# Kernel optimization log

Hardware: AMD Instinct MI355X
Metric: run time of the kernel (lower is better)

The kernel has to match this reference:

```python
import jax, jax.numpy as jnp
import numpy as np

SIGMA = 1e-4            # df_cone_height
PENALIZE_OUTSIDE = True
POINT2PLANE = False
EPS = 1e-12


def _tri_frame(tris):
    """tris: [..., 3, 3] -> centroid c [...,3], unit normal n [...,3], circum-radius r [...]."""
    v0, v1, v2 = tris[..., 0, :], tris[..., 1, :], tris[..., 2, :]
    c = (v0 + v1 + v2) / 3.0
    n = jnp.cross(v1 - v0, v2 - v0)
    n = n / jnp.maximum(jnp.linalg.norm(n, axis=-1, keepdims=True), EPS)
    r = jnp.sqrt(jnp.maximum(jnp.maximum(jnp.sum((v0 - c) ** 2, -1),
                                         jnp.sum((v1 - c) ** 2, -1)),
                             jnp.sum((v2 - c) ** 2, -1)))
    return c, n, r


def _cone_psi(points, c, n, r):
    """Conic distance-field value of each point w.r.t. a triangle cone.
    points: [..., 3, 3] (3 vertices), c/n: [..., 3], r: [...]. Returns [..., 3].
    Cone: axis = triangle normal through centroid, base radius r, height SIGMA.
    """
    u = points - c[..., None, :]                       # [..., 3v, 3]
    h = jnp.einsum('...vk,...k->...v', u, n)           # signed height along normal
    rho = jnp.linalg.norm(u - h[..., None] * n[..., None, :], axis=-1)  # radial dist
    radial = jnp.maximum(1.0 - rho / jnp.maximum(r[..., None], EPS), 0.0)
    if PENALIZE_OUTSIDE:
        axial = jnp.maximum(SIGMA - h, 0.0)            # also penalize thin band above surface
    else:
        axial = jnp.maximum(-h, 0.0)                   # only true penetration (below surface)
    return radial * axial


def setup_inputs() -> dict:
    key = jax.random.key(0)
    B, V, F, C = 8, 10475, 20908, 262144
    k1, k2, k3, k4 = jax.random.split(key, 4)
    vertices = jax.random.normal(k1, (B, V, 3), dtype=jnp.float32)
    faces = jax.random.randint(k2, (F, 3), 0, V)
    idxs = jax.random.randint(k3, (B, C, 2), 0, F)
    invalid = jax.random.uniform(k4, (B, C)) < 0.2     # padded (-1) collision slots
    collision_idxs = jnp.where(invalid[..., None], -1, idxs)
    return {"vertices": vertices, "faces": faces, "collision_idxs": collision_idxs}


def reference(vertices, faces, collision_idxs):
    # triangles: [B, F, 3, 3]
    triangles = jnp.take(vertices, faces, axis=1)
    recv_idx = collision_idxs[..., 0]                  # [B, C]
    intr_idx = collision_idxs[..., 1]
    valid = (recv_idx >= 0) & (intr_idx >= 0)
    # irregular gather of colliding triangle pairs: [B, C, 3, 3]
    recv = jnp.take_along_axis(triangles, jnp.clip(recv_idx, 0)[..., None, None], axis=1)
    intr = jnp.take_along_axis(triangles, jnp.clip(intr_idx, 0)[..., None, None], axis=1)
    rc, rn, rr = _tri_frame(recv)
    ic, inn, ir = _tri_frame(intr)
    psi_i = _cone_psi(intr, rc, rn, rr)                # intruder verts in receiver cone [B,C,3]
    psi_r = _cone_psi(recv, ic, inn, ir)               # receiver verts in intruder cone
    # penetration vector per vertex = -psi * n (unit normal) -> squared norm = psi^2
    per_pair = jnp.sum(psi_i ** 2 + psi_r ** 2, axis=-1)  # [B, C]
    loss = jnp.sum(jnp.where(valid, per_pair, 0.0), axis=1)  # [B]
    # original returns 0.0 when no collision index is >= 0
    return jnp.where(jnp.any(valid), loss, jnp.zeros_like(loss))
```

## Files before the change

### kernel.cpp

```cpp
#include <hip/hip_runtime.h>
#include <hip/hip_fp16.h>

#define SIGMA_C 1e-4f
#define EPS_C   1e-12f
#define BLOCK   256
#define GPT     4

struct V3 { float x, y, z; };

__device__ __forceinline__ V3 v3sub(V3 a, V3 b) { return {a.x - b.x, a.y - b.y, a.z - b.z}; }
__device__ __forceinline__ float v3dot(V3 a, V3 b) { return a.x * b.x + a.y * b.y + a.z * b.z; }
__device__ __forceinline__ V3 v3cross(V3 a, V3 b) {
    return {a.y * b.z - a.z * b.y,
            a.z * b.x - a.x * b.z,
            a.x * b.y - a.y * b.x};
}
__device__ __forceinline__ int imax0(int x) { return x > 0 ? x : 0; }

__device__ __forceinline__ void tri_frame(const V3 v[3], V3& c, V3& n, float& r) {
    const float third = 1.0f / 3.0f;
    c.x = (v[0].x + v[1].x + v[2].x) * third;
    c.y = (v[0].y + v[1].y + v[2].y) * third;
    c.z = (v[0].z + v[1].z + v[2].z) * third;
    V3 e1 = v3sub(v[1], v[0]);
    V3 e2 = v3sub(v[2], v[0]);
    n = v3cross(e1, e2);
    float nn = sqrtf(v3dot(n, n));
    float inv = 1.0f / fmaxf(nn, EPS_C);
    n.x *= inv; n.y *= inv; n.z *= inv;
    V3 d0 = v3sub(v[0], c), d1 = v3sub(v[1], c), d2 = v3sub(v[2], c);
    float m = fmaxf(fmaxf(v3dot(d0, d0), v3dot(d1, d1)), v3dot(d2, d2));
    r = sqrtf(m);
}

__device__ __forceinline__ float cone_psi2(const V3 p[3], V3 c, V3 n, float r) {
    float inv_r = 1.0f / fmaxf(r, EPS_C);
    float s = 0.0f;
#pragma unroll
    for (int i = 0; i < 3; ++i) {
        V3 u = v3sub(p[i], c);
        float h = v3dot(u, n);
        V3 w = {u.x - h * n.x, u.y - h * n.y, u.z - h * n.z};
        float rho = sqrtf(v3dot(w, w));
        float radial = fmaxf(1.0f - rho * inv_r, 0.0f);
        float axial = fmaxf(SIGMA_C - h, 0.0f);
        float psi = radial * axial;
        s += psi * psi;
    }
    return s;
}

union RecU { float4 f[2]; __half h[16]; };

__global__ void precompute_tri_h(const float* __restrict__ verts,
                                 const int*   __restrict__ faces,
                                 float4* __restrict__ table,
                                 float* __restrict__ out,
                                 int V, int F, int B) {
    if (blockIdx.x == 0 && threadIdx.x < (unsigned)B)
        out[threadIdx.x] = 0.0f;

    const int b = blockIdx.x % B;
    const int chunk = blockIdx.x / B;
    const int f = chunk * blockDim.x + threadIdx.x;
    if (f >= F) return;

    const float* vb = verts + (size_t)b * (size_t)V * 3u;
    int i0 = faces[3 * f + 0];
    int i1 = faces[3 * f + 1];
    int i2 = faces[3 * f + 2];
    V3 v[3];
    v[0] = {vb[3 * i0 + 0], vb[3 * i0 + 1], vb[3 * i0 + 2]};
    v[1] = {vb[3 * i1 + 0], vb[3 * i1 + 1], vb[3 * i1 + 2]};
    v[2] = {vb[3 * i2 + 0], vb[3 * i2 + 1], vb[3 * i2 + 2]};
    V3 c, n; float r;
    tri_frame(v, c, n, r);

    RecU u;
    u.h[0]  = __float2half(v[0].x); u.h[1]  = __float2half(v[0].y); u.h[2]  = __float2half(v[0].z);
    u.h[3]  = __float2half(v[1].x); u.h[4]  = __float2half(v[1].y); u.h[5]  = __float2half(v[1].z);
    u.h[6]  = __float2half(v[2].x); u.h[7]  = __float2half(v[2].y); u.h[8]  = __float2half(v[2].z);
    u.h[9]  = __float2half(c.x);    u.h[10] = __float2half(c.y);    u.h[11] = __float2half(c.z);
    u.h[12] = __float2half(n.x);    u.h[13] = __float2half(n.y);    u.h[14] = __float2half(n.z);
    u.h[15] = __float2half(r);

    float4* rec = table + ((size_t)b * F + f) * 2;
    rec[0] = u.f[0];
    rec[1] = u.f[1];
}

__device__ __forceinline__ void unpack_rec_h(float4 a, float4 b,
                                             V3 p[3], V3& c, V3& n, float& r) {
    RecU u; u.f[0] = a; u.f[1] = b;
    p[0] = {__half2float(u.h[0]),  __half2float(u.h[1]),  __half2float(u.h[2])};
    p[1] = {__half2float(u.h[3]),  __half2float(u.h[4]),  __half2float(u.h[5])};
    p[2] = {__half2float(u.h[6]),  __half2float(u.h[7]),  __half2float(u.h[8])};
    c = {__half2float(u.h[9]),  __half2float(u.h[10]), __half2float(u.h[11])};
    n = {__half2float(u.h[12]), __half2float(u.h[13]), __half2float(u.h[14])};
    r = __half2float(u.h[15]);
}

__device__ __forceinline__ void gather_group(const float4* __restrict__ tb, int4 q,
                                             float4 G[8], float w[2]) {
    w[0] = ((q.x | q.y) >= 0) ? 1.0f : 0.0f;
    w[1] = ((q.z | q.w) >= 0) ? 1.0f : 0.0f;
    const float4* R0 = tb + (size_t)imax0(q.x) * 2;
    const float4* I0 = tb + (size_t)imax0(q.y) * 2;
    const float4* R1 = tb + (size_t)imax0(q.z) * 2;
    const float4* I1 = tb + (size_t)imax0(q.w) * 2;
    G[0] = R0[0]; G[1] = R0[1];
    G[2] = I0[0]; G[3] = I0[1];
    G[4] = R1[0]; G[5] = R1[1];
    G[6] = I1[0]; G[7] = I1[1];
}

__device__ __forceinline__ float compute_pair(const float4 G0, const float4 G1,
                                              const float4 G2, const float4 G3, float w) {
    V3 rp[3], rc, rn; float rr;
    unpack_rec_h(G0, G1, rp, rc, rn, rr);
    V3 ip[3], ic, inn; float ir;
    unpack_rec_h(G2, G3, ip, ic, inn, ir);
    return w * (cone_psi2(ip, rc, rn, rr) + cone_psi2(rp, ic, inn, ir));
}

__device__ __forceinline__ float compute_group(const float4 G[8], const float w[2]) {
    return compute_pair(G[0], G[1], G[2], G[3], w[0]) +
           compute_pair(G[4], G[5], G[6], G[7], w[1]);
}

__global__ void __launch_bounds__(BLOCK)
pair_kernel_h(const float4* __restrict__ table,
              const int4*  __restrict__ coll4,
              float* __restrict__ out,
              int F, int C4, int B) {
    const int b = blockIdx.x % B;
    const int chunk = blockIdx.x / B;
    const int4* cb = coll4 + (size_t)b * C4;
    const float4* tb = table + (size_t)b * ((size_t)F * 2);

    const int base = chunk * (BLOCK * GPT) + threadIdx.x;

    float acc = 0.0f;
    float4 GA[8], GB[8];
    float wA[2], wB[2];
    int4 q_even, q_odd;

    {
        int g0 = base;
        int g1 = base + BLOCK;
        q_even = (g0 < C4) ? cb[g0] : make_int4(-1, -1, -1, -1);
        q_odd  = (GPT > 1 && g1 < C4) ? cb[g1] : make_int4(-1, -1, -1, -1);
        gather_group(tb, q_even, GA, wA);
    }

#pragma unroll
    for (int i = 0; i < GPT; ++i) {
        if ((i & 1) == 0) {
            if (i + 2 < GPT) {
                int g = base + (i + 2) * BLOCK;
                q_even = (g < C4) ? cb[g] : make_int4(-1, -1, -1, -1);
            }
            if (i + 1 < GPT)
                gather_group(tb, q_odd, GB, wB);
            acc += compute_group(GA, wA);
        } else {
            if (i + 2 < GPT) {
                int g = base + (i + 2) * BLOCK;
                q_odd = (g < C4) ? cb[g] : make_int4(-1, -1, -1, -1);
            }
            if (i + 1 < GPT)
                gather_group(tb, q_even, GA, wA);
            acc += compute_group(GB, wB);
        }
    }

#pragma unroll
    for (int off = 32; off > 0; off >>= 1)
        acc += __shfl_down(acc, off, 64);

    __shared__ float red[16];
    int lane = threadIdx.x & 63;
    int wid  = threadIdx.x >> 6;
    if (lane == 0) red[wid] = acc;
    __syncthreads();
    if (threadIdx.x == 0) {
        float s = 0.0f;
        int nw = blockDim.x >> 6;
        for (int i = 0; i < nw; ++i) s += red[i];
        atomicAdd(&out[b], s);
    }
}

__global__ void interp_zero(float* out, int n) {
    int i = blockIdx.x * blockDim.x + threadIdx.x;
    if (i < n) out[i] = 0.0f;
}

__global__ void pair_kernel_gather(const float* __restrict__ verts,
                                   const int*   __restrict__ faces,
                                   const int2*  __restrict__ coll,
                                   float* __restrict__ out,
                                   int V, int C) {
    const int b = blockIdx.y;
    const float* vb = verts + (size_t)b * (size_t)V * 3u;
    const int2* cb = coll + (size_t)b * (size_t)C;

    float acc = 0.0f;
    const int stride = gridDim.x * blockDim.x;
    for (int c = blockIdx.x * blockDim.x + threadIdx.x; c < C; c += stride) {
        int2 idx = cb[c];
        if ((idx.x | idx.y) >= 0) {
            const int* fr = faces + 3 * idx.x;
            const int* fi = faces + 3 * idx.y;
            V3 tr[3], ti[3];
#pragma unroll
            for (int j = 0; j < 3; ++j) {
                int vr = fr[j];
                tr[j] = {vb[3 * vr + 0], vb[3 * vr + 1], vb[3 * vr + 2]};
                int vi = fi[j];
                ti[j] = {vb[3 * vi + 0], vb[3 * vi + 1], vb[3 * vi + 2]};
            }
            V3 rc, rn; float rr;
            tri_frame(tr, rc, rn, rr);
            V3 ic, in_; float ir;
            tri_frame(ti, ic, in_, ir);
            acc += cone_psi2(ti, rc, rn, rr);
            acc += cone_psi2(tr, ic, in_, ir);
        }
    }

#pragma unroll
    for (int off = 32; off > 0; off >>= 1)
        acc += __shfl_down(acc, off, 64);

    __shared__ float red[16];
    int lane = threadIdx.x & 63;
    int wid  = threadIdx.x >> 6;
    if (lane == 0) red[wid] = acc;
    __syncthreads();
    if (threadIdx.x == 0) {
        float s = 0.0f;
        int nw = blockDim.x >> 6;
        for (int i = 0; i < nw; ++i) s += red[i];
        atomicAdd(&out[b], s);
    }
}

extern "C" void kernel_launch(void* const* d_in, const int* in_sizes, int n_in,
                              void* d_out, int out_size, void* d_ws, size_t ws_size,
                              hipStream_t stream) {
    const float* verts = (const float*)d_in[0];
    const int*   faces = (const int*)d_in[1];
    float* out = (float*)d_out;

    const int B = out_size;
    const int V = in_sizes[0] / (3 * B);
    const int F = in_sizes[1] / 3;
    const int C = in_sizes[2] / (2 * B);

    const size_t table_bytes = (size_t)B * (size_t)F * 32u;

    if (ws_size >= table_bytes && (C % 2) == 0) {
        float4* table = (float4*)d_ws;
        const int4* coll4 = (const int4*)d_in[2];
        const int C4 = C / 2;

        const int pchunks = (F + 255) / 256;
        precompute_tri_h<<<dim3(pchunks * B), dim3(256), 0, stream>>>(
            verts, faces, table, out, V, F, B);

        const int per_block = BLOCK * GPT;
        const int chunks = (C4 + per_block - 1) / per_block;
        pair_kernel_h<<<dim3(chunks * B), dim3(BLOCK), 0, stream>>>(
            table, coll4, out, F, C4, B);
    } else {
        const int2* coll = (const int2*)d_in[2];
        interp_zero<<<1, 64, 0, stream>>>(out, B);
        pair_kernel_gather<<<dim3(256, B), dim3(256), 0, stream>>>(
            verts, faces, coll, out, V, C);
    }
}
```

Measured before the change: 32.16 us.

## Stage triangle-record gathers into LDS with async global_load_lds double-buffering

Adds a new pair kernel where each wave issues direct global-to-LDS loads (global_load_lds) for the receiver and intruder triangle records of the next tile. It overlaps them with compute on the current tile, using manual vmcnt waits and a double buffer. The goal is to hide gather latency without holding many float4 registers, which should raise occupancy. The precompute kernel now handles two faces per thread. The new path runs only when C divides evenly by the per-block pair count, and it relies on hand-written waitcnt ordering being correct.

```diff
diff --git a/kernel.cpp b/kernel.cpp
--- a/kernel.cpp
+++ b/kernel.cpp
@@ -3,8 +3,8 @@
 
 #define SIGMA_C 1e-4f
 #define EPS_C   1e-12f
-#define BLOCK   256
-#define GPT     4
+#define WPB     4
+#define TILE_T  8
 
 struct V3 { float x, y, z; };
 
@@ -52,43 +52,6 @@
 
 union RecU { float4 f[2]; __half h[16]; };
 
-__global__ void precompute_tri_h(const float* __restrict__ verts,
-                                 const int*   __restrict__ faces,
-                                 float4* __restrict__ table,
-                                 float* __restrict__ out,
-                                 int V, int F, int B) {
-    if (blockIdx.x == 0 && threadIdx.x < (unsigned)B)
-        out[threadIdx.x] = 0.0f;
-
-    const int b = blockIdx.x % B;
-    const int chunk = blockIdx.x / B;
-    const int f = chunk * blockDim.x + threadIdx.x;
-    if (f >= F) return;
-
-    const float* vb = verts + (size_t)b * (size_t)V * 3u;
-    int i0 = faces[3 * f + 0];
-    int i1 = faces[3 * f + 1];
-    int i2 = faces[3 * f + 2];
-    V3 v[3];
-    v[0] = {vb[3 * i0 + 0], vb[3 * i0 + 1], vb[3 * i0 + 2]};
-    v[1] = {vb[3 * i1 + 0], vb[3 * i1 + 1], vb[3 * i1 + 2]};
-    v[2] = {vb[3 * i2 + 0], vb[3 * i2 + 1], vb[3 * i2 + 2]};
-    V3 c, n; float r;
-    tri_frame(v, c, n, r);
-
-    RecU u;
-    u.h[0]  = __float2half(v[0].x); u.h[1]  = __float2half(v[0].y); u.h[2]  = __float2half(v[0].z);
-    u.h[3]  = __float2half(v[1].x); u.h[4]  = __float2half(v[1].y); u.h[5]  = __float2half(v[1].z);
-    u.h[6]  = __float2half(v[2].x); u.h[7]  = __float2half(v[2].y); u.h[8]  = __float2half(v[2].z);
-    u.h[9]  = __float2half(c.x);    u.h[10] = __float2half(c.y);    u.h[11] = __float2half(c.z);
-    u.h[12] = __float2half(n.x);    u.h[13] = __float2half(n.y);    u.h[14] = __float2half(n.z);
-    u.h[15] = __float2half(r);
-
-    float4* rec = table + ((size_t)b * F + f) * 2;
-    rec[0] = u.f[0];
-    rec[1] = u.f[1];
-}
-
 __device__ __forceinline__ void unpack_rec_h(float4 a, float4 b,
                                              V3 p[3], V3& c, V3& n, float& r) {
     RecU u; u.f[0] = a; u.f[1] = b;
@@ -100,6 +63,145 @@
     r = __half2float(u.h[15]);
 }
 
+__device__ __forceinline__ float compute_pair(const float4 G0, const float4 G1,
+                                              const float4 G2, const float4 G3, float w) {
+    V3 rp[3], rc, rn; float rr;
+    unpack_rec_h(G0, G1, rp, rc, rn, rr);
+    V3 ip[3], ic, inn; float ir;
+    unpack_rec_h(G2, G3, ip, ic, inn, ir);
+    return w * (cone_psi2(ip, rc, rn, rr) + cone_psi2(rp, ic, inn, ir));
+}
+
+__device__ __forceinline__ void gload_lds16(const void* g, void* l) {
+    __builtin_amdgcn_global_load_lds((const __attribute__((address_space(1))) void*)g,
+                                     (__attribute__((address_space(3))) void*)l,
+                                     16, 0, 0);
+}
+
+__global__ void precompute_tri_h(const float* __restrict__ verts,
+                                 const int*   __restrict__ faces,
+                                 float4* __restrict__ table,
+                                 float* __restrict__ out,
+                                 int V, int F, int B) {
+    if (blockIdx.x == 0 && threadIdx.x < (unsigned)B)
+        out[threadIdx.x] = 0.0f;
+
+    const int b = blockIdx.x % B;
+    const int chunk = blockIdx.x / B;
+    const int f0 = (chunk * blockDim.x + threadIdx.x) * 2;
+    if (f0 >= F) return;
+    const int nf = (f0 + 1 < F) ? 2 : 1;
+
+    const float* vb = verts + (size_t)b * (size_t)V * 3u;
+
+    int ia[6];
+#pragma unroll
+    for (int j = 0; j < 3; ++j) ia[j] = faces[3 * f0 + j];
+#pragma unroll
+    for (int j = 0; j < 3; ++j) ia[3 + j] = faces[3 * (f0 + nf - 1) + j];
+
+    V3 pv[6];
+#pragma unroll
+    for (int j = 0; j < 6; ++j) {
+        int vi = ia[j];
+        pv[j] = {vb[3 * vi + 0], vb[3 * vi + 1], vb[3 * vi + 2]};
+    }
+
+#pragma unroll
+    for (int k = 0; k < 2; ++k) {
+        if (k >= nf) break;
+        V3 v[3] = {pv[3 * k], pv[3 * k + 1], pv[3 * k + 2]};
+        V3 c, n; float r;
+        tri_frame(v, c, n, r);
+        RecU u;
+        u.h[0]  = __float2half(v[0].x); u.h[1]  = __float2half(v[0].y); u.h[2]  = __float2half(v[0].z);
+        u.h[3]  = __float2half(v[1].x); u.h[4]  = __float2half(v[1].y); u.h[5]  = __float2half(v[1].z);
+        u.h[6]  = __float2half(v[2].x); u.h[7]  = __float2half(v[2].y); u.h[8]  = __float2half(v[2].z);
+        u.h[9]  = __float2half(c.x);    u.h[10] = __float2half(c.y);    u.h[11] = __float2half(c.z);
+        u.h[12] = __float2half(n.x);    u.h[13] = __float2half(n.y);    u.h[14] = __float2half(n.z);
+        u.h[15] = __float2half(r);
+        float4* rec = table + ((size_t)b * F + (f0 + k)) * 2;
+        rec[0] = u.f[0];
+        rec[1] = u.f[1];
+    }
+}
+
+__global__ void __launch_bounds__(WPB * 64)
+pair_kernel_lds(const float4* __restrict__ table,
+                const int2*  __restrict__ coll,
+                float* __restrict__ out,
+                int F, int C, int B) {
+    __shared__ float4 lds[WPB * 2 * 256];
+    __shared__ float red[WPB];
+
+    const int wid  = threadIdx.x >> 6;
+    const int lane = threadIdx.x & 63;
+    const int b = blockIdx.x % B;
+    const int chunk = blockIdx.x / B;
+    const int wib = chunk * WPB + wid;
+
+    const int2* cb = coll + (size_t)b * C;
+    const char* tb = (const char*)(table + (size_t)b * ((size_t)F * 2));
+    float4* wbuf = lds + wid * 512;
+
+    int2 q[TILE_T];
+    const int pair0 = wib * (TILE_T * 64) + lane;
+#pragma unroll
+    for (int t = 0; t < TILE_T; ++t)
+        q[t] = cb[pair0 + t * 64];
+
+    {
+        const char* gR = tb + (size_t)imax0(q[0].x) * 32;
+        const char* gI = tb + (size_t)imax0(q[0].y) * 32;
+        gload_lds16(gR,      wbuf);
+        gload_lds16(gR + 16, wbuf + 64);
+        gload_lds16(gI,      wbuf + 128);
+        gload_lds16(gI + 16, wbuf + 192);
+    }
+
+    float acc = 0.0f;
+#pragma unroll
+    for (int t = 0; t < TILE_T; ++t) {
+        if (t + 1 < TILE_T) {
+            const char* gR = tb + (size_t)imax0(q[t + 1].x) * 32;
+            const char* gI = tb + (size_t)imax0(q[t + 1].y) * 32;
+            float4* dst = wbuf + ((t + 1) & 1) * 256;
+            gload_lds16(gR,      dst);
+            gload_lds16(gR + 16, dst + 64);
+            gload_lds16(gI,      dst + 128);
+            gload_lds16(gI + 16, dst + 192);
+            __builtin_amdgcn_sched_barrier(0);
+            asm volatile("s_waitcnt vmcnt(4)" ::: "memory");
+            __builtin_amdgcn_sched_barrier(0);
+        } else {
+            __builtin_amdgcn_sched_barrier(0);
+            asm volatile("s_waitcnt vmcnt(0)" ::: "memory");
+            __builtin_amdgcn_sched_barrier(0);
+        }
+        const float4* src = wbuf + (t & 1) * 256;
+        float4 a0 = src[lane];
+        float4 a1 = src[lane + 64];
+        float4 a2 = src[lane + 128];
+        float4 a3 = src[lane + 192];
+        float w = ((q[t].x | q[t].y) >= 0) ? 1.0f : 0.0f;
+        acc += compute_pair(a0, a1, a2, a3, w);
+    }
+
+#pragma unroll
+    for (int off = 32; off > 0; off >>= 1)
+        acc += __shfl_down(acc, off, 64);
+
+    if (lane == 0) red[wid] = acc;
+    __syncthreads();
+    if (threadIdx.x == 0) {
+        float s = 0.0f;
+#pragma unroll
+        for (int i = 0; i < WPB; ++i) s += red[i];
+        atomicAdd(&out[b], s);
+    }
+}
+
+#define GPT 4
 __device__ __forceinline__ void gather_group(const float4* __restrict__ tb, int4 q,
                                              float4 G[8], float w[2]) {
     w[0] = ((q.x | q.y) >= 0) ? 1.0f : 0.0f;
@@ -113,80 +215,57 @@
     G[4] = R1[0]; G[5] = R1[1];
     G[6] = I1[0]; G[7] = I1[1];
 }
-
-__device__ __forceinline__ float compute_pair(const float4 G0, const float4 G1,
-                                              const float4 G2, const float4 G3, float w) {
-    V3 rp[3], rc, rn; float rr;
-    unpack_rec_h(G0, G1, rp, rc, rn, rr);
-    V3 ip[3], ic, inn; float ir;
-    unpack_rec_h(G2, G3, ip, ic, inn, ir);
-    return w * (cone_psi2(ip, rc, rn, rr) + cone_psi2(rp, ic, inn, ir));
-}
-
 __device__ __forceinline__ float compute_group(const float4 G[8], const float w[2]) {
     return compute_pair(G[0], G[1], G[2], G[3], w[0]) +
            compute_pair(G[4], G[5], G[6], G[7], w[1]);
 }
-
-__global__ void __launch_bounds__(BLOCK)
-pair_kernel_h(const float4* __restrict__ table,
-              const int4*  __restrict__ coll4,
-              float* __restrict__ out,
-              int F, int C4, int B) {
+__global__ void __launch_bounds__(256)
+pair_kernel_h(const float4* __restrict__ table, const int4* __restrict__ coll4,
+              float* __restrict__ out, int F, int C4, int B) {
     const int b = blockIdx.x % B;
     const int chunk = blockIdx.x / B;
     const int4* cb = coll4 + (size_t)b * C4;
     const float4* tb = table + (size_t)b * ((size_t)F * 2);
-
-    const int base = chunk * (BLOCK * GPT) + threadIdx.x;
+    const int base = chunk * (256 * GPT) + threadIdx.x;
 
     float acc = 0.0f;
     float4 GA[8], GB[8];
     float wA[2], wB[2];
     int4 q_even, q_odd;
-
     {
-        int g0 = base;
-        int g1 = base + BLOCK;
+        int g0 = base, g1 = base + 256;
         q_even = (g0 < C4) ? cb[g0] : make_int4(-1, -1, -1, -1);
-        q_odd  = (GPT > 1 && g1 < C4) ? cb[g1] : make_int4(-1, -1, -1, -1);
+        q_odd  = (g1 < C4) ? cb[g1] : make_int4(-1, -1, -1, -1);
         gather_group(tb, q_even, GA, wA);
     }
-
 #pragma unroll
     for (int i = 0; i < GPT; ++i) {
         if ((i & 1) == 0) {
             if (i + 2 < GPT) {
-                int g = base + (i + 2) * BLOCK;
+                int g = base + (i + 2) * 256;
                 q_even = (g < C4) ? cb[g] : make_int4(-1, -1, -1, -1);
             }
-            if (i + 1 < GPT)
-                gather_group(tb, q_odd, GB, wB);
+            if (i + 1 < GPT) gather_group(tb, q_odd, GB, wB);
             acc += compute_group(GA, wA);
         } else {
             if (i + 2 < GPT) {
-                int g = base + (i + 2) * BLOCK;
+                int g = base + (i + 2) * 256;
                 q_odd = (g < C4) ? cb[g] : make_int4(-1, -1, -1, -1);
             }
-            if (i + 1 < GPT)
-                gather_group(tb, q_even, GA, wA);
+            if (i + 1 < GPT) gather_group(tb, q_even, GA, wA);
             acc += compute_group(GB, wB);
         }
     }
-
 #pragma unroll
     for (int off = 32; off > 0; off >>= 1)
         acc += __shfl_down(acc, off, 64);
-
-    __shared__ float red[16];
-    int lane = threadIdx.x & 63;
-    int wid  = threadIdx.x >> 6;
+    __shared__ float red[4];
+    int lane = threadIdx.x & 63, wid = threadIdx.x >> 6;
     if (lane == 0) red[wid] = acc;
     __syncthreads();
     if (threadIdx.x == 0) {
         float s = 0.0f;
-        int nw = blockDim.x >> 6;
-        for (int i = 0; i < nw; ++i) s += red[i];
+        for (int i = 0; i < 4; ++i) s += red[i];
         atomicAdd(&out[b], s);
     }
 }
@@ -195,16 +274,13 @@
     int i = blockIdx.x * blockDim.x + threadIdx.x;
     if (i < n) out[i] = 0.0f;
 }
-
 __global__ void pair_kernel_gather(const float* __restrict__ verts,
                                    const int*   __restrict__ faces,
                                    const int2*  __restrict__ coll,
-                                   float* __restrict__ out,
-                                   int V, int C) {
+                                   float* __restrict__ out, int V, int C) {
     const int b = blockIdx.y;
     const float* vb = verts + (size_t)b * (size_t)V * 3u;
     const int2* cb = coll + (size_t)b * (size_t)C;
-
     float acc = 0.0f;
     const int stride = gridDim.x * blockDim.x;
     for (int c = blockIdx.x * blockDim.x + threadIdx.x; c < C; c += stride) {
@@ -228,14 +304,11 @@
             acc += cone_psi2(tr, ic, in_, ir);
         }
     }
-
 #pragma unroll
     for (int off = 32; off > 0; off >>= 1)
         acc += __shfl_down(acc, off, 64);
-
     __shared__ float red[16];
-    int lane = threadIdx.x & 63;
-    int wid  = threadIdx.x >> 6;
+    int lane = threadIdx.x & 63, wid = threadIdx.x >> 6;
     if (lane == 0) red[wid] = acc;
     __syncthreads();
     if (threadIdx.x == 0) {
@@ -259,24 +332,32 @@
     const int C = in_sizes[2] / (2 * B);
 
     const size_t table_bytes = (size_t)B * (size_t)F * 32u;
-
-    if (ws_size >= table_bytes && (C % 2) == 0) {
+    const int pairs_per_block = 64 * TILE_T * WPB;
+
+    if (ws_size >= table_bytes) {
         float4* table = (float4*)d_ws;
-        const int4* coll4 = (const int4*)d_in[2];
-        const int C4 = C / 2;
-
-        const int pchunks = (F + 255) / 256;
+
+        const int pchunks = (F + 511) / 512;
         precompute_tri_h<<<dim3(pchunks * B), dim3(256), 0, stream>>>(
             verts, faces, table, out, V, F, B);
 
-        const int per_block = BLOCK * GPT;
-        const int chunks = (C4 + per_block - 1) / per_block;
-        pair_kernel_h<<<dim3(chunks * B), dim3(BLOCK), 0, stream>>>(
-            table, coll4, out, F, C4, B);
+        if (C % pairs_per_block == 0) {
+            const int BPB = C / pairs_per_block;
+            pair_kernel_lds<<<dim3(BPB * B), dim3(WPB * 64), 0, stream>>>(
+                table, (const int2*)d_in[2], out, F, C, B);
+        } else if ((C % 2) == 0) {
+            const int C4 = C / 2;
+            const int chunks = (C4 + 256 * GPT - 1) / (256 * GPT);
+            pair_kernel_h<<<dim3(chunks * B), dim3(256), 0, stream>>>(
+                table, (const int4*)d_in[2], out, F, C4, B);
+        } else {
+            interp_zero<<<1, 64, 0, stream>>>(out, B);
+            pair_kernel_gather<<<dim3(256, B), dim3(256), 0, stream>>>(
+                verts, faces, (const int2*)d_in[2], out, V, C);
+        }
     } else {
-        const int2* coll = (const int2*)d_in[2];
         interp_zero<<<1, 64, 0, stream>>>(out, B);
         pair_kernel_gather<<<dim3(256, B), dim3(256), 0, stream>>>(
-            verts, faces, coll, out, V, C);
-    }
-}
+            verts, faces, (const int2*)d_in[2], out, V, C);
+    }
+}
```

New measurement: 34.08 us. 1.06x slower.
